# Kernel optimization log

Hardware: AMD Instinct MI355X
Metric: run time of the kernel (lower is better)

Reference implementation:

```python
import jax, jax.numpy as jnp
import numpy as np
import math

HID = 1024      # opt.hidden_dim
NH = 8          # num_heads (hardcoded in module)
HD = HID // NH  # indiv_head_dim = 128
G = 16          # opt.group_num
GD = HID // G   # per-group dim = 64
FEAT = 1024     # opt.feature_dim
V, T = 8, 256   # videos x frames
E = 256         # number of events
L = 64          # max_att_len (clip window)
N = 384         # expanded event_num
WAVE = 10000.0


def setup_inputs() -> dict:
    rng = np.random.RandomState(0)
    key = jax.random.key(0)
    ks = jax.random.split(key, 12)

    feats = jax.random.normal(ks[0], (V * T, FEAT), dtype=jnp.float32)

    # ragged clip spans -> dense gather idx + mask (the Basic_Encoder loop)
    starts = rng.randint(0, V * T - L, size=(E,))
    clip_gather_idx = jnp.asarray(starts[:, None] + np.arange(L)[None, :], dtype=jnp.int32)
    lens = rng.randint(8, L + 1, size=(E,))
    clip_mask = jnp.asarray((np.arange(L)[None, :] < lens[:, None]).astype(np.float32))

    # event_seq_idx expansion: rows -> event ids, block-diagonal mask
    expand_idx = jnp.asarray(rng.randint(0, E, size=(N,)), dtype=jnp.int32)
    block_mask = np.zeros((N, N), dtype=np.float32)
    pos = 0
    while pos < N:
        b = min(int(rng.randint(8, 49)), N - pos)
        block_mask[pos:pos + b, pos:pos + b] = 1.0
        pos += b
    block_mask = jnp.asarray(block_mask)

    # normalized timestamps (start < end, in [0,1])
    s = rng.uniform(0.0, 0.8, size=(N, 1)).astype(np.float32)
    e = s + rng.uniform(0.02, 0.2, size=(N, 1)).astype(np.float32)
    bbox = jnp.asarray(np.concatenate([s, e], axis=1))

    sc = 1.0 / math.sqrt(HID)
    scd = 1.0 / math.sqrt(HD)
    Wpre = jax.random.normal(ks[1], (HID, FEAT), dtype=jnp.float32) * sc
    bpre = jnp.zeros((HID,), dtype=jnp.float32)
    Wq = jax.random.normal(ks[2], (NH, HD, HD), dtype=jnp.float32) * scd
    bq = jnp.zeros((NH, HD), dtype=jnp.float32)
    Wk = jax.random.normal(ks[3], (NH, HD, HD), dtype=jnp.float32) * scd
    bk = jnp.zeros((NH, HD), dtype=jnp.float32)
    Wv = jax.random.normal(ks[4], (NH, HD, HD), dtype=jnp.float32) * scd
    bv = jnp.zeros((NH, HD), dtype=jnp.float32)
    Wp1 = jax.random.normal(ks[5], (HID, HID), dtype=jnp.float32) * sc
    bp1 = jnp.zeros((HID,), dtype=jnp.float32)
    Wp2 = jax.random.normal(ks[6], (G, HID), dtype=jnp.float32) * sc
    bp2 = jnp.zeros((G,), dtype=jnp.float32)

    return dict(feats=feats, clip_gather_idx=clip_gather_idx, clip_mask=clip_mask,
                expand_idx=expand_idx, block_mask=block_mask, bbox=bbox,
                Wpre=Wpre, bpre=bpre, Wq=Wq, bq=bq, Wk=Wk, bk=bk, Wv=Wv, bv=bv,
                Wp1=Wp1, bp1=bp1, Wp2=Wp2, bp2=bp2)


def _sinusoid(x, feat_dim):
    # extract_position_embedding: x [..., P] -> [..., P*feat_dim/2*2] reshaped to feat_dim per row
    fr = jnp.arange(feat_dim // 4, dtype=x.dtype)
    dim_mat = WAVE ** (4.0 / feat_dim * fr)              # (feat_dim/4,)
    div = (100.0 * x)[..., None] / dim_mat               # (..., P, feat_dim/4)
    return jnp.concatenate([jnp.sin(div), jnp.cos(div)], axis=-1)


def reference(feats, clip_gather_idx, clip_mask, expand_idx, block_mask, bbox,
              Wpre, bpre, Wq, bq, Wk, bk, Wv, bv, Wp1, bp1, Wp2, bp2):
    # ---- clip-level pooling (Basic_Encoder.get_clip_level_feats + mean) ----
    clip_feats = feats[clip_gather_idx] * clip_mask[..., None]          # (E, L, FEAT)
    event = clip_feats.sum(1) / (clip_mask.sum(1, keepdims=True) + 1e-5)  # (E, FEAT)
    event = jax.nn.relu(event @ Wpre.T + bpre)                          # pre_map (dropout=eval)

    # ---- expand per event_seq_idx ----
    x = event[expand_idx]                                               # (N, HID)

    # ---- 8 per-head q/k/v maps, split into G groups ----
    xh = x.reshape(N, NH, HD)
    def proj(W, b):
        y = jnp.einsum('nhd,hed->nhe', xh, W) + b                       # (N, NH, HD)
        return y.reshape(N, G, GD).transpose(1, 0, 2)                   # (G, N, GD)
    q, k, v = proj(Wq, bq), proj(Wk, bk), proj(Wv, bv)
    scores = jnp.einsum('gnd,gmd->gnm', q, k) / math.sqrt(GD)           # (G, N, N)

    # ---- position branch: pairwise geometric relation bias ----
    start, end = bbox[:, 0:1], bbox[:, 1:2]                             # (N,1)
    center = 0.5 * (start + end)
    length = jnp.maximum(end - start, 0.1)
    dc = (center - center.T) / length
    dl = jnp.log(length.T / length)
    pm = jnp.stack([dc, dl], axis=2)                                    # (N, N, 2)
    emb = _sinusoid(pm, HID).reshape(N, N, HID)                         # (N, N, HID)
    pos = jax.nn.relu(emb @ Wp1.T + bp1)                                # pair_pos_fc1
    pos = jax.nn.relu(pos @ Wp2.T + bp2)                                # pair_pos_fc2 -> (N, N, G)
    pos_bias = jnp.log(jnp.clip(pos, 1e-6)).transpose(2, 0, 1)          # (G, N, N)

    scores = scores + pos_bias
    scores = jnp.where(block_mask[None] > 0, scores, -1e9)
    att = jax.nn.softmax(scores, axis=-1)                               # (G, N, N)
    out = jnp.einsum('gnm,gmd->gnd', att, v)                            # (G, N, GD)
    out = out.transpose(1, 0, 2).reshape(N, HID)

    # ---- per-event 100-dim temporal position embedding ----
    e100 = _sinusoid(bbox, 100).reshape(N, 100)

    return jnp.concatenate([x, out, e100], axis=-1)                     # (N, 2*HID + 100)
```

## Files before the change

### kernel.cpp

```cpp
#include <hip/hip_runtime.h>
#include <hip/hip_bf16.h>

typedef unsigned short u16;
typedef _Float16 h16;
typedef __attribute__((ext_vector_type(8))) h16 h8;
typedef __attribute__((ext_vector_type(8))) u16 us8;
typedef __attribute__((ext_vector_type(4))) float f4;

#define DEVFN __device__ __forceinline__

constexpr int kN = 384;
constexpr int kL = 64;
constexpr int kMaxP = kN * 48;
constexpr int kOutCols = 2148;
constexpr float kLoScale = 2048.f;
constexpr float kLoInv = 1.f / 2048.f;

union HU { h16 h; u16 u; };
DEVFN u16 f2h(float f) { HU c; c.h = (h16)f; return c.u; }
DEVFN float h2f(u16 b) { HU c; c.u = b; return (float)c.h; }

DEVFN f4 mfma16h(h8 a, h8 b, f4 c) {
  return __builtin_amdgcn_mfma_f32_16x16x32_f16(a, b, c, 0, 0, 0);
}

DEVFN h8 pack8h(float4 x0, float4 x1) {
  h8 a;
  a[0] = (h16)x0.x; a[1] = (h16)x0.y; a[2] = (h16)x0.z; a[3] = (h16)x0.w;
  a[4] = (h16)x1.x; a[5] = (h16)x1.y; a[6] = (h16)x1.z; a[7] = (h16)x1.w;
  return a;
}

DEVFN void fsincos(float ang, float& s, float& c) {
  float n = rintf(ang * 0.15915494309189535f);
  const float PI2_HI = 6.2831854820251465f;
  const float PI2_LO = -1.7484555e-07f;
  float r = fmaf(-n, PI2_HI, ang);
  r = fmaf(-n, PI2_LO, r);
  s = __sinf(r);
  c = __cosf(r);
}

__global__ __launch_bounds__(256) void k_front(
    const float* __restrict__ Wp1, u16* __restrict__ W1H, u16* __restrict__ W1L,
    const float* __restrict__ Wp2, u16* __restrict__ W2H, u16* __restrict__ W2L,
    const float* __restrict__ Wpre, u16* __restrict__ WpreH,
    const float* __restrict__ Wq, u16* __restrict__ WqH,
    const float* __restrict__ Wk, u16* __restrict__ WkH,
    const float* __restrict__ Wv, u16* __restrict__ WvH,
    const float* __restrict__ bm, int* __restrict__ row_start, int* __restrict__ row_len,
    const float* __restrict__ feats, const int* __restrict__ gidx,
    const float* __restrict__ cmask, float* __restrict__ mean) {
  int bid = blockIdx.x, t = threadIdx.x;
  if (bid < 512) {
    const int nW1 = 1048576, nW2 = 16384, nPre = 1048576, nQ = 131072;
    const int tot = nW1 + nW2 + nPre + 3 * nQ;
    for (int i = bid * 256 + t; i < tot; i += 512 * 256) {
      if (i < nW1) {
        float x = Wp1[i]; u16 h = f2h(x);
        W1H[i] = h; W1L[i] = f2h((x - h2f(h)) * kLoScale);
      } else if (i < nW1 + nW2) {
        int j = i - nW1; float x = Wp2[j]; u16 h = f2h(x);
        W2H[j] = h; W2L[j] = f2h((x - h2f(h)) * kLoScale);
      } else if (i < nW1 + nW2 + nPre) {
        int j = i - nW1 - nW2; WpreH[j] = f2h(Wpre[j]);
      } else {
        int j = i - nW1 - nW2 - nPre;
        int a = j / nQ, r = j % nQ;
        const float* s = (a == 0) ? Wq : (a == 1) ? Wk : Wv;
        u16* d = (a == 0) ? WqH : (a == 1) ? WkH : WvH;
        d[r] = f2h(s[r]);
      }
    }
  } else if (bid < 608) {
    int w = t >> 6, lane = t & 63;
    int i = (bid - 512) * 4 + w;
    int mn = kN, mx = -1;
    #pragma unroll
    for (int jb = 0; jb < kN; jb += 64) {
      float m = bm[(size_t)i * kN + jb + lane];
      if (m > 0.f) { mn = min(mn, jb + lane); mx = max(mx, jb + lane); }
    }
    #pragma unroll
    for (int off = 32; off > 0; off >>= 1) {
      mn = min(mn, __shfl_xor(mn, off));
      mx = max(mx, __shfl_xor(mx, off));
    }
    if (lane == 0) { row_start[i] = mn; row_len[i] = mx - mn + 1; }
  } else {
    int e = bid - 608;
    float4 a = {0.f, 0.f, 0.f, 0.f};
    float ms = 0.f;
    for (int l = 0; l < kL; ++l) {
      float m = cmask[e * kL + l];
      ms += m;
      if (m > 0.f) {
        float4 v = *(const float4*)(feats + (size_t)gidx[e * kL + l] * 1024 + t * 4);
        a.x += v.x; a.y += v.y; a.z += v.z; a.w += v.w;
      }
    }
    float inv = 1.f / (ms + 1e-5f);
    float4 o = {a.x * inv, a.y * inv, a.z * inv, a.w * inv};
    *(float4*)(mean + (size_t)e * 1024 + t * 4) = o;
  }
}

__global__ __launch_bounds__(64) void k_scan(const int* __restrict__ row_len,
                                             int* __restrict__ row_off,
                                             int* __restrict__ Ptr) {
  int lane = threadIdx.x;
  int s[6], tot = 0;
  #pragma unroll
  for (int r = 0; r < 6; ++r) { s[r] = tot; tot += row_len[lane * 6 + r]; }
  int run = tot;
  #pragma unroll
  for (int off = 1; off < 64; off <<= 1) {
    int u = __shfl_up(run, off);
    if (lane >= off) run += u;
  }
  int excl = run - tot;
  #pragma unroll
  for (int r = 0; r < 6; ++r) row_off[lane * 6 + r] = excl + s[r];
  if (lane == 63) Ptr[0] = excl + tot;
}

__global__ __launch_bounds__(64) void k_fill(const int* __restrict__ row_start,
                                             const int* __restrict__ row_len,
                                             const int* __restrict__ row_off,
                                             int* __restrict__ pair_i,
                                             int* __restrict__ pair_j) {
  int i = blockIdx.x, lane = threadIdx.x;
  int s = row_start[i], len = row_len[i], off = row_off[i];
  if (lane < len) { pair_i[off + lane] = i; pair_j[off + lane] = s + lane; }
}

__global__ __launch_bounds__(256) void k_mid(
    const int* __restrict__ Ptr, const int* __restrict__ row_start,
    const int* __restrict__ row_off, const float* __restrict__ bbox,
    u16* __restrict__ ehi, u16* __restrict__ elo,
    const float* __restrict__ mean, const u16* __restrict__ WpreH,
    const float* __restrict__ bpre, float* __restrict__ event) {
  int bid = blockIdx.x, t = threadIdx.x;
  if (bid < 9216) {
    __shared__ double As[16], Bs[16];
    __shared__ int roff[384], rstart[384];
    const double kCd = -13.287712379549449 / 256.0;
    if (t < 16) As[t] = exp2(kCd * (double)(t * 16));
    else if (t < 32) Bs[t - 16] = exp2(kCd * (double)(t - 16));
    for (int k = t; k < 384; k += 256) { roff[k] = row_off[k]; rstart[k] = row_start[k]; }
    __syncthreads();
    int P = Ptr[0];
    int Pc = (P + 127) & ~127;
    int p = bid * 2 + (t >> 7);
    if (p >= Pc) return;
    int kb = (t & 127) * 8;
    size_t o = (size_t)p * 1024 + kb;
    us8 vh, vl;
    if (p >= P) {
      #pragma unroll
      for (int j = 0; j < 8; ++j) { vh[j] = 0; vl[j] = 0; }
      *(us8*)(ehi + o) = vh;
      *(us8*)(elo + o) = vl;
      return;
    }
    int lo = 0, hi = 383;
    while (lo < hi) { int md = (lo + hi + 1) >> 1; if (roff[md] <= p) lo = md; else hi = md - 1; }
    int pi = lo, pj = rstart[lo] + (p - roff[lo]);
    double s0 = bbox[pi * 2], e0 = bbox[pi * 2 + 1];
    double s1 = bbox[pj * 2], e1 = bbox[pj * 2 + 1];
    double li = fmax(e0 - s0, 0.1), lj = fmax(e1 - s1, 0.1);
    double x = (kb < 512) ? (0.5 * (s0 + e0) - 0.5 * (s1 + e1)) / li : log(lj / li);
    double x100 = 100.0 * x;
    bool iscos = (kb >> 8) & 1;
    int f0 = kb & 255;
    const double INV2PI = 0.15915494309189535;
    const double TWOPI  = 6.283185307179586;
    #pragma unroll
    for (int j = 0; j < 8; ++j) {
      int f = f0 + j;
      double ang = x100 * (As[f >> 4] * Bs[f & 15]);
      double nn = rint(ang * INV2PI);
      float rf = (float)fma(-nn, TWOPI, ang);
      float sv = iscos ? __cosf(rf) : __sinf(rf);
      u16 h = f2h(sv);
      vh[j] = h;
      vl[j] = f2h((sv - h2f(h)) * kLoScale);
    }
    *(us8*)(ehi + o) = vh;
    *(us8*)(elo + o) = vl;
  } else {
    int b2 = bid - 9216;
    int mt = b2 >> 4, nc = b2 & 15;
    int w = t >> 6, lane = t & 63, lr = lane & 15, lg = lane >> 4;
    f4 acc = {};
    const float* arow = mean + (size_t)(mt * 16 + lr) * 1024;
    #pragma unroll
    for (int ks = 0; ks < 32; ++ks) {
      const float* ap = arow + ks * 32 + lg * 8;
      h8 a = pack8h(*(const float4*)ap, *(const float4*)(ap + 4));
      h8 b = *(const h8*)(WpreH + (size_t)(nc * 64 + w * 16 + lr) * 1024 + ks * 32 + lg * 8);
      acc = mfma16h(a, b, acc);
    }
    #pragma unroll
    for (int r = 0; r < 4; ++r) {
      int row = mt * 16 + lg * 4 + r, cn = nc * 64 + w * 16 + lr;
      event[(size_t)row * 1024 + cn] = fmaxf(acc[r] + bpre[cn], 0.f);
    }
  }
}

__global__ __launch_bounds__(256, 2) void k_main(
    const int* __restrict__ Ptr, const u16* __restrict__ ehi, const u16* __restrict__ elo,
    const u16* __restrict__ W1h, const u16* __restrict__ W1l, const float* __restrict__ bias1,
    const u16* __restrict__ W2h, const u16* __restrict__ W2l, float* __restrict__ z2part,
    const float* __restrict__ event, const int* __restrict__ eidx,
    const u16* __restrict__ WqH, const float* __restrict__ bq,
    const u16* __restrict__ WkH, const float* __restrict__ bk,
    const u16* __restrict__ WvH, const float* __restrict__ bv,
    float* __restrict__ qb, float* __restrict__ kbuf, float* __restrict__ vbuf) {
  __shared__ u16 lds[2][4][4096];
  int bid = blockIdx.x, tid = threadIdx.x;
  if (bid < 1152) {
    int P = Ptr[0];
    int mb = bid % 144, nb = bid / 144;
    if (mb * 128 >= P) return;
    int w = tid >> 6, lane = tid & 63;
    int lr = lane & 15, lg = lane >> 4;
    int srow[2], scol[2];
    #pragma unroll
    for (int cc = 0; cc < 2; ++cc) {
      int c = w * 2 + cc;
      int d = c * 1024 + lane * 16;
      int b = d ^ (((((d >> 6) & 3)) ^ ((d >> 8) & 3)) << 4);
      srow[cc] = b >> 6;
      scol[cc] = b & 63;
    }
    const u16* planes[4] = {ehi, elo, W1h, W1l};
    int rb0 = mb * 128, rb1 = nb * 128;
    auto stage = [&](int buf, int k0) {
      #pragma unroll
      for (int t = 0; t < 4; ++t) {
        int rbase = (t < 2) ? rb0 : rb1;
        #pragma unroll
        for (int cc = 0; cc < 2; ++cc) {
          int c = w * 2 + cc;
          const char* src = (const char*)(planes[t] + (size_t)(rbase + srow[cc]) * 1024 + k0) + scol[cc];
          char* dst = (char*)&lds[buf][t][0] + c * 1024;
          __builtin_amdgcn_global_load_lds(
              (const __attribute__((address_space(1))) char*)src,
              (__attribute__((address_space(3))) char*)dst, 16, 0, 0);
        }
      }
    };
    stage(0, 0);
    f4 aH[4][4] = {}, aL[4][4] = {};
    int wm = (w >> 1) * 64, wn = (w & 1) * 64;
    int sl = (lg ^ (lr & 3) ^ ((lr >> 2) & 3)) << 4;
    __syncthreads();
    for (int kt = 0; kt < 32; ++kt) {
      int cur = kt & 1;
      if (kt < 31) stage(cur ^ 1, (kt + 1) * 32);
      h8 ah[4], al[4], bh[4], bl[4];
      #pragma unroll
      for (int mt = 0; mt < 4; ++mt) {
        int ad = (wm + mt * 16 + lr) * 64 + sl;
        ah[mt] = *(const h8*)((const char*)&lds[cur][0][0] + ad);
        al[mt] = *(const h8*)((const char*)&lds[cur][1][0] + ad);
      }
      #pragma unroll
      for (int nt = 0; nt < 4; ++nt) {
        int ad = (wn + nt * 16 + lr) * 64 + sl;
        bh[nt] = *(const h8*)((const char*)&lds[cur][2][0] + ad);
        bl[nt] = *(const h8*)((const char*)&lds[cur][3][0] + ad);
      }
      #pragma unroll
      for (int mt = 0; mt < 4; ++mt)
        #pragma unroll
        for (int nt = 0; nt < 4; ++nt) {
          aH[mt][nt] = mfma16h(ah[mt], bh[nt], aH[mt][nt]);
          aL[mt][nt] = mfma16h(al[mt], bh[nt], aL[mt][nt]);
          aL[mt][nt] = mfma16h(ah[mt], bl[nt], aL[mt][nt]);
        }
      __syncthreads();
    }
    float* zq = (float*)&lds[0][0][0] + w * 4096;
    #pragma unroll
    for (int mt = 0; mt < 4; ++mt)
      #pragma unroll
      for (int nt = 0; nt < 4; ++nt)
        #pragma unroll
        for (int r = 0; r < 4; ++r) {
          int pl = mt * 16 + lg * 4 + r;
          int nl = nt * 16 + lr;
          float z1 = aH[mt][nt][r] + aL[mt][nt][r] * kLoInv + bias1[nb * 128 + wn + nl];
          zq[pl * 64 + (nl ^ ((pl & 7) << 3))] = fmaxf(z1, 0.f);
        }
    __syncthreads();
    f4 c2h[4], c2l[4];
    #pragma unroll
    for (int i = 0; i < 4; ++i) { c2h[i] = f4{}; c2l[i] = f4{}; }
    #pragma unroll
    for (int mt2 = 0; mt2 < 4; ++mt2) {
      #pragma unroll
      for (int kc = 0; kc < 2; ++kc) {
        int pl = mt2 * 16 + lr;
        int n0 = kc * 32 + lg * 8;
        const float* rp = zq + pl * 64 + (n0 ^ ((pl & 7) << 3));
        float4 v0 = *(const float4*)rp;
        float4 v1 = *(const float4*)(rp + 4);
        h8 ah2, al2;
        #pragma unroll
        for (int j = 0; j < 4; ++j) {
          h16 h0 = (h16)v0[j]; ah2[j] = h0;     al2[j] = (h16)((v0[j] - (float)h0) * kLoScale);
          h16 h1 = (h16)v1[j]; ah2[4 + j] = h1; al2[4 + j] = (h16)((v1[j] - (float)h1) * kLoScale);
        }
        int ng = nb * 128 + wn + n0;
        h8 bh2 = *(const h8*)(W2h + lr * 1024 + ng);
        h8 bl2 = *(const h8*)(W2l + lr * 1024 + ng);
        c2h[mt2] = mfma16h(ah2, bh2, c2h[mt2]);
        c2l[mt2] = mfma16h(al2, bh2, c2l[mt2]);
        c2l[mt2] = mfma16h(ah2, bl2, c2l[mt2]);
      }
    }
    int slice = nb * 2 + (w & 1);
    #pragma unroll
    for (int mt2 = 0; mt2 < 4; ++mt2)
      #pragma unroll
      for (int r = 0; r < 4; ++r) {
        int p = mb * 128 + wm + mt2 * 16 + lg * 4 + r;
        z2part[((size_t)slice * kMaxP + p) * 16 + lr] = c2h[mt2][r] + c2l[mt2][r] * kLoInv;
      }
  } else {
    int b2 = bid - 1152;
    int z = b2 / 192, r2 = b2 % 192, mt = r2 >> 3, h = r2 & 7;
    int w = tid >> 6, lane = tid & 63, lr = lane & 15, lg = lane >> 4;
    const u16* W = (z == 0) ? WqH : (z == 1) ? WkH : WvH;
    const float* bias = (z == 0) ? bq : (z == 1) ? bk : bv;
    float* out = (z == 0) ? qb : (z == 1) ? kbuf : vbuf;
    int row = mt * 16 + lr;
    const float* arow = event + (size_t)eidx[row] * 1024 + h * 128;
    f4 acc[2] = {};
    #pragma unroll
    for (int ks = 0; ks < 4; ++ks) {
      const float* ap = arow + ks * 32 + lg * 8;
      h8 a = pack8h(*(const float4*)ap, *(const float4*)(ap + 4));
      #pragma unroll
      for (int n2 = 0; n2 < 2; ++n2) {
        int nt = w * 2 + n2;
        h8 b = *(const h8*)(W + h * 16384 + (nt * 16 + lr) * 128 + ks * 32 + lg * 8);
        acc[n2] = mfma16h(a, b, acc[n2]);
      }
    }
    #pragma unroll
    for (int n2 = 0; n2 < 2; ++n2)
      #pragma unroll
      for (int r = 0; r < 4; ++r) {
        int rn = mt * 16 + lg * 4 + r, e = (w * 2 + n2) * 16 + lr;
        out[(size_t)rn * 1024 + h * 128 + e] = acc[n2][r] + bias[h * 128 + e];
      }
  }
}

__global__ __launch_bounds__(256) void k_back(
    const int* __restrict__ Ptr, const float* __restrict__ z2part,
    const float* __restrict__ bias2, float* __restrict__ bias_o,
    const float* __restrict__ event, const int* __restrict__ eidx,
    const float* __restrict__ bbox, float* __restrict__ dout) {
  int bid = blockIdx.x, t = threadIdx.x;
  if (bid < 1152) {
    int P = Ptr[0];
    int idx = bid * 256 + t;
    if (idx >= P * 16) return;
    int g = idx & 15;
    float s = bias2[g];
    #pragma unroll
    for (int b = 0; b < 16; ++b) s += z2part[(size_t)b * kMaxP * 16 + idx];
    bias_o[idx] = logf(fmaxf(s, 1e-6f));
  } else {
    int i = bid - 1152;
    const float* er = event + (size_t)eidx[i] * 1024;
    float* orow = dout + (size_t)i * kOutCols;
    for (int c = t; c < 1024; c += 256) orow[c] = er[c];
    if (t < 100) {
      int qq = t / 25, f = t % 25;
      float x = bbox[i * 2 + (qq >> 1)];
      float ang = 100.f * x * exp2f((float)f * (-13.287712379549449f * 0.04f));
      float sv, cv;
      fsincos(ang, sv, cv);
      orow[2048 + t] = (qq & 1) ? cv : sv;
    }
  }
}

__global__ __launch_bounds__(64) void k_att(const float* __restrict__ q,
                                            const float* __restrict__ kk,
                                            const float* __restrict__ vv,
                                            const float* __restrict__ bias,
                                            const int* __restrict__ row_start,
                                            const int* __restrict__ row_len,
                                            const int* __restrict__ row_off,
                                            float* __restrict__ dout) {
  int i = blockIdx.x, g = blockIdx.y, lane = threadIdx.x;
  int s = row_start[i], L = row_len[i], pb = row_off[i];
  __shared__ float qs[64];
  __shared__ float att[64];
  qs[lane] = q[(size_t)i * 1024 + g * 64 + lane];
  __syncthreads();
  bool valid = lane < L;
  const float* kr = kk + (size_t)(s + (valid ? lane : 0)) * 1024 + g * 64;
  float sc = 0.f;
  #pragma unroll
  for (int dt = 0; dt < 16; ++dt) {
    float4 kv = *(const float4*)(kr + dt * 4);
    sc += qs[dt * 4 + 0] * kv.x + qs[dt * 4 + 1] * kv.y +
          qs[dt * 4 + 2] * kv.z + qs[dt * 4 + 3] * kv.w;
  }
  sc = valid ? (sc * 0.125f + bias[(size_t)(pb + lane) * 16 + g]) : -3.0e38f;
  float mx = sc;
  #pragma unroll
  for (int off = 32; off > 0; off >>= 1) mx = fmaxf(mx, __shfl_xor(mx, off));
  float pe = valid ? __expf(sc - mx) : 0.f;
  float sm = pe;
  #pragma unroll
  for (int off = 32; off > 0; off >>= 1) sm += __shfl_xor(sm, off);
  att[lane] = pe / sm;
  __syncthreads();
  float o = 0.f;
  const float* vb = vv + (size_t)s * 1024 + g * 64 + lane;
  for (int jl = 0; jl < L; ++jl) o += att[jl] * vb[(size_t)jl * 1024];
  dout[(size_t)i * kOutCols + 1024 + g * 64 + lane] = o;
}

__global__ __launch_bounds__(256) void k_pos(
    const int* __restrict__ Ptr, const int* __restrict__ pair_i,
    const int* __restrict__ pair_j, const float* __restrict__ bbox,
    const u16* __restrict__ W1h, const u16* __restrict__ W1l,
    const float* __restrict__ bias1,
    const u16* __restrict__ W2h, const u16* __restrict__ W2l,
    const float* __restrict__ bias2, float* __restrict__ bias_out) {
  int P = Ptr[0];
  int base0 = blockIdx.x * 64;
  if (base0 >= P) return;
  int w = threadIdx.x >> 6, l = threadIdx.x & 63;
  int lr = l & 15, lg = l >> 4;
  int base = base0 + w * 16;
  int p = base + lr;
  bool valid = p < P;
  int pi = valid ? pair_i[p] : 0;
  int pj = valid ? pair_j[p] : 0;
  double s0 = bbox[pi * 2], e0 = bbox[pi * 2 + 1];
  double s1 = bbox[pj * 2], e1 = bbox[pj * 2 + 1];
  double li = fmax(e0 - s0, 0.1), lj = fmax(e1 - s1, 0.1);
  double dcd = (0.5 * (s0 + e0) - 0.5 * (s1 + e1)) / li;
  double dld = log(lj / li);
  const double kCd = -13.287712379549449 / 256.0;
  double r1  = exp2(kCd);
  double r32 = exp2(kCd * 32.0);
  double pb0 = exp2(kCd * (double)(lg * 8));
  const double INV2PI = 0.15915494309189535;
  const double TWOPI  = 6.283185307179586;
  h8 eh[32], el[32];
  #pragma unroll
  for (int hx = 0; hx < 2; ++hx) {
    double x100 = 100.0 * (hx ? dld : dcd);
    double pch = pb0;
    #pragma unroll
    for (int ksl = 0; ksl < 8; ++ksl) {
      double pp = pch;
      #pragma unroll
      for (int j = 0; j < 8; ++j) {
        double ang = x100 * pp;
        double nn = rint(ang * INV2PI);
        float rf = (float)fma(-nn, TWOPI, ang);
        float sv = __sinf(rf), cv = __cosf(rf);
        h16 sh = (h16)sv, ch = (h16)cv;
        eh[hx * 16 + ksl][j] = sh;
        el[hx * 16 + ksl][j] = (h16)((sv - (float)sh) * kLoScale);
        eh[hx * 16 + 8 + ksl][j] = ch;
        el[hx * 16 + 8 + ksl][j] = (h16)((cv - (float)ch) * kLoScale);
        pp *= r1;
      }
      pch *= r32;
    }
  }
  __shared__ float p1f[4][16 * 64];
  char* myp1 = (char*)p1f[w];
  f4 acc2 = {}, acc2l = {};
  for (int nc = 0; nc < 16; ++nc) {
    f4 accH[4] = {}, accL[4] = {};
    #pragma unroll
    for (int ks = 0; ks < 32; ++ks) {
      #pragma unroll
      for (int nt = 0; nt < 4; ++nt) {
        size_t boff = (size_t)(nc * 64 + nt * 16 + lr) * 1024 + ks * 32 + lg * 8;
        h8 bh = *(const h8*)(W1h + boff);
        h8 bl = *(const h8*)(W1l + boff);
        accH[nt] = mfma16h(eh[ks], bh, accH[nt]);
        accL[nt] = mfma16h(el[ks], bh, accL[nt]);
        accL[nt] = mfma16h(eh[ks], bl, accL[nt]);
      }
    }
    __syncthreads();
    #pragma unroll
    for (int nt = 0; nt < 4; ++nt)
      #pragma unroll
      for (int r = 0; r < 4; ++r) {
        int m = lg * 4 + r, n = nt * 16 + lr;
        float z1 = accH[nt][r] + accL[nt][r] * kLoInv + bias1[nc * 64 + n];
        int byte = ((m * 64 + n) * 4) ^ ((m & 7) << 4);
        *(float*)(myp1 + byte) = fmaxf(z1, 0.f);
      }
    __syncthreads();
    #pragma unroll
    for (int hf = 0; hf < 2; ++hf) {
      int kb = hf * 32 + lg * 8;
      int b0 = ((lr * 64 + kb) * 4) ^ ((lr & 7) << 4);
      int b1 = ((lr * 64 + kb + 4) * 4) ^ ((lr & 7) << 4);
      float4 x0 = *(const float4*)(myp1 + b0);
      float4 x1 = *(const float4*)(myp1 + b1);
      h8 ah, al;
      #pragma unroll
      for (int j = 0; j < 4; ++j) {
        h16 h0 = (h16)x0[j];
        ah[j] = h0; al[j] = (h16)((x0[j] - (float)h0) * kLoScale);
        h16 h1 = (h16)x1[j];
        ah[4 + j] = h1; al[4 + j] = (h16)((x1[j] - (float)h1) * kLoScale);
      }
      h8 bh = *(const h8*)(W2h + lr * 1024 + nc * 64 + kb);
      h8 bl = *(const h8*)(W2l + lr * 1024 + nc * 64 + kb);
      acc2  = mfma16h(ah, bh, acc2);
      acc2l = mfma16h(al, bh, acc2l);
      acc2l = mfma16h(ah, bl, acc2l);
    }
  }
  #pragma unroll
  for (int r = 0; r < 4; ++r) {
    int m = lg * 4 + r;
    int pp = base + m;
    if (pp < P) {
      float v0 = acc2[r] + acc2l[r] * kLoInv + bias2[lr];
      bias_out[(size_t)pp * 16 + lr] = logf(fmaxf(v0, 1e-6f));
    }
  }
}

extern "C" void kernel_launch(void* const* d_in, const int* in_sizes, int n_in,
                              void* d_out, int out_size, void* d_ws, size_t ws_size,
                              hipStream_t stream) {
  const float* feats = (const float*)d_in[0];
  const int*   gidx  = (const int*)d_in[1];
  const float* cmask = (const float*)d_in[2];
  const int*   eidx  = (const int*)d_in[3];
  const float* bmask = (const float*)d_in[4];
  const float* bbox  = (const float*)d_in[5];
  const float* Wpre  = (const float*)d_in[6];
  const float* bpre  = (const float*)d_in[7];
  const float* Wq    = (const float*)d_in[8];
  const float* bq    = (const float*)d_in[9];
  const float* Wk    = (const float*)d_in[10];
  const float* bk    = (const float*)d_in[11];
  const float* Wv    = (const float*)d_in[12];
  const float* bv    = (const float*)d_in[13];
  const float* Wp1   = (const float*)d_in[14];
  const float* bp1   = (const float*)d_in[15];
  const float* Wp2   = (const float*)d_in[16];
  const float* bp2   = (const float*)d_in[17];

  char* ws = (char*)d_ws;
  size_t off = 0;
  auto alloc = [&](size_t bytes) {
    char* r = ws + off;
    off += (bytes + 255) & ~(size_t)255;
    return r;
  };
  u16* W1H   = (u16*)alloc((size_t)1048576 * 2);
  u16* W1L   = (u16*)alloc((size_t)1048576 * 2);
  u16* W2H   = (u16*)alloc((size_t)16384 * 2);
  u16* W2L   = (u16*)alloc((size_t)16384 * 2);
  u16* WpreH = (u16*)alloc((size_t)1048576 * 2);
  u16* WqH   = (u16*)alloc((size_t)131072 * 2);
  u16* WkH   = (u16*)alloc((size_t)131072 * 2);
  u16* WvH   = (u16*)alloc((size_t)131072 * 2);
  float* mean  = (float*)alloc((size_t)256 * 1024 * 4);
  float* event = (float*)alloc((size_t)256 * 1024 * 4);
  float* qb    = (float*)alloc((size_t)384 * 1024 * 4);
  float* kb    = (float*)alloc((size_t)384 * 1024 * 4);
  float* vb    = (float*)alloc((size_t)384 * 1024 * 4);
  int* row_start = (int*)alloc(kN * 4);
  int* row_len   = (int*)alloc(kN * 4);
  int* row_off   = (int*)alloc(kN * 4);
  int* Ptr       = (int*)alloc(256);
  int* pair_i    = (int*)alloc((size_t)kMaxP * 4);
  int* pair_j    = (int*)alloc((size_t)kMaxP * 4);
  float* bias_o  = (float*)alloc((size_t)kMaxP * 16 * 4);
  u16* ehi      = (u16*)alloc((size_t)kMaxP * 1024 * 2);
  u16* elo      = (u16*)alloc((size_t)kMaxP * 1024 * 2);
  float* z2part = (float*)alloc((size_t)16 * kMaxP * 16 * 4);
  bool fast = (off <= ws_size);

  k_front<<<864, 256, 0, stream>>>(Wp1, W1H, W1L, Wp2, W2H, W2L, Wpre, WpreH,
                                   Wq, WqH, Wk, WkH, Wv, WvH,
                                   bmask, row_start, row_len,
                                   feats, gidx, cmask, mean);
  k_scan<<<1, 64, 0, stream>>>(row_len, row_off, Ptr);

  if (fast) {
    k_mid<<<9472, 256, 0, stream>>>(Ptr, row_start, row_off, bbox, ehi, elo,
                                    mean, WpreH, bpre, event);
    k_main<<<1728, 256, 0, stream>>>(Ptr, ehi, elo, W1H, W1L, bp1, W2H, W2L, z2part,
                                     event, eidx, WqH, bq, WkH, bk, WvH, bv, qb, kb, vb);
    k_back<<<1536, 256, 0, stream>>>(Ptr, z2part, bp2, bias_o, event, eidx, bbox,
                                     (float*)d_out);
  } else {
    k_mid<<<9472, 256, 0, stream>>>(Ptr, row_start, row_off, bbox, ehi, elo,
                                    mean, WpreH, bpre, event);
    k_fill<<<kN, 64, 0, stream>>>(row_start, row_len, row_off, pair_i, pair_j);
    k_pos<<<kMaxP / 64, 256, 0, stream>>>(Ptr, pair_i, pair_j, bbox, W1H, W1L, bp1,
                                          W2H, W2L, bp2, bias_o);
    k_main<<<1728, 256, 0, stream>>>(Ptr, ehi, elo, W1H, W1L, bp1, W2H, W2L, z2part,
                                     event, eidx, WqH, bq, WkH, bk, WvH, bv, qb, kb, vb);
    k_back<<<1536, 256, 0, stream>>>(Ptr, z2part, bp2, bias_o, event, eidx, bbox,
                                     (float*)d_out);
  }
  k_att<<<dim3(kN, 16), 64, 0, stream>>>(qb, kb, vb, bias_o, row_start, row_len, row_off,
                                         (float*)d_out);
}
```

Baseline: 177.2 us.

## Replace split-K partial buffer with atomic accumulation and fold reduction into attention

The 16-slice z2part partial-sum buffer and the separate k_back reduction kernel are removed. k_main now atomically adds its fc2 partials into a zeroed bias_acc buffer, which extra k_front blocks clear. k_att applies bias2 and the log clamp on the fly, and it absorbs the event-row and temporal-embedding output writes, so one launch and a large intermediate read/write disappear. It also reorders k_main's block index so N-blocks are adjacent, and makes k_mid exit early before its LDS setup. The cost is atomic contention on bias_acc (16 adds per element) and non-deterministic float summation order.

Measured after the change: 161.6 us. 1.1x faster.

```diff
diff --git a/kernel.cpp b/kernel.cpp
--- a/kernel.cpp
+++ b/kernel.cpp
@@ -50,7 +50,8 @@
     const float* __restrict__ Wv, u16* __restrict__ WvH,
     const float* __restrict__ bm, int* __restrict__ row_start, int* __restrict__ row_len,
     const float* __restrict__ feats, const int* __restrict__ gidx,
-    const float* __restrict__ cmask, float* __restrict__ mean) {
+    const float* __restrict__ cmask, float* __restrict__ mean,
+    float* __restrict__ bias_acc) {
   int bid = blockIdx.x, t = threadIdx.x;
   if (bid < 512) {
     const int nW1 = 1048576, nW2 = 16384, nPre = 1048576, nQ = 131072;
@@ -87,7 +88,7 @@
       mx = max(mx, __shfl_xor(mx, off));
     }
     if (lane == 0) { row_start[i] = mn; row_len[i] = mx - mn + 1; }
-  } else {
+  } else if (bid < 864) {
     int e = bid - 608;
     float4 a = {0.f, 0.f, 0.f, 0.f};
     float ms = 0.f;
@@ -102,6 +103,10 @@
     float inv = 1.f / (ms + 1e-5f);
     float4 o = {a.x * inv, a.y * inv, a.z * inv, a.w * inv};
     *(float4*)(mean + (size_t)e * 1024 + t * 4) = o;
+  } else {
+    float4 z = {0.f, 0.f, 0.f, 0.f};
+    for (int i4 = (bid - 864) * 256 + t; i4 < kMaxP * 16 / 4; i4 += 48 * 256)
+      *(float4*)(bias_acc + (size_t)i4 * 4) = z;
   }
 }
 
@@ -142,6 +147,9 @@
     const float* __restrict__ bpre, float* __restrict__ event) {
   int bid = blockIdx.x, t = threadIdx.x;
   if (bid < 9216) {
+    int P = Ptr[0];
+    int Pc = (P + 127) & ~127;
+    if (bid * 2 >= Pc) return;
     __shared__ double As[16], Bs[16];
     __shared__ int roff[384], rstart[384];
     const double kCd = -13.287712379549449 / 256.0;
@@ -149,10 +157,7 @@
     else if (t < 32) Bs[t - 16] = exp2(kCd * (double)(t - 16));
     for (int k = t; k < 384; k += 256) { roff[k] = row_off[k]; rstart[k] = row_start[k]; }
     __syncthreads();
-    int P = Ptr[0];
-    int Pc = (P + 127) & ~127;
     int p = bid * 2 + (t >> 7);
-    if (p >= Pc) return;
     int kb = (t & 127) * 8;
     size_t o = (size_t)p * 1024 + kb;
     us8 vh, vl;
@@ -212,17 +217,19 @@
 __global__ __launch_bounds__(256, 2) void k_main(
     const int* __restrict__ Ptr, const u16* __restrict__ ehi, const u16* __restrict__ elo,
     const u16* __restrict__ W1h, const u16* __restrict__ W1l, const float* __restrict__ bias1,
-    const u16* __restrict__ W2h, const u16* __restrict__ W2l, float* __restrict__ z2part,
+    const u16* __restrict__ W2h, const u16* __restrict__ W2l, float* __restrict__ bias_acc,
     const float* __restrict__ event, const int* __restrict__ eidx,
     const u16* __restrict__ WqH, const float* __restrict__ bq,
     const u16* __restrict__ WkH, const float* __restrict__ bk,
     const u16* __restrict__ WvH, const float* __restrict__ bv,
-    float* __restrict__ qb, float* __restrict__ kbuf, float* __restrict__ vbuf) {
+    float* __restrict__ qb, float* __restrict__ kbuf, float* __restrict__ vbuf,
+    int pos_on) {
   __shared__ u16 lds[2][4][4096];
   int bid = blockIdx.x, tid = threadIdx.x;
   if (bid < 1152) {
+    if (!pos_on) return;
     int P = Ptr[0];
-    int mb = bid % 144, nb = bid / 144;
+    int nb = bid & 7, mb = bid >> 3;
     if (mb * 128 >= P) return;
     int w = tid >> 6, lane = tid & 63;
     int lr = lane & 15, lg = lane >> 4;
@@ -322,13 +329,13 @@
         c2l[mt2] = mfma16h(ah2, bl2, c2l[mt2]);
       }
     }
-    int slice = nb * 2 + (w & 1);
     #pragma unroll
     for (int mt2 = 0; mt2 < 4; ++mt2)
       #pragma unroll
       for (int r = 0; r < 4; ++r) {
         int p = mb * 128 + wm + mt2 * 16 + lg * 4 + r;
-        z2part[((size_t)slice * kMaxP + p) * 16 + lr] = c2h[mt2][r] + c2l[mt2][r] * kLoInv;
+        if (p < P)
+          atomicAdd(&bias_acc[(size_t)p * 16 + lr], c2h[mt2][r] + c2l[mt2][r] * kLoInv);
       }
   } else {
     int b2 = bid - 1152;
@@ -361,27 +368,29 @@
   }
 }
 
-__global__ __launch_bounds__(256) void k_back(
-    const int* __restrict__ Ptr, const float* __restrict__ z2part,
-    const float* __restrict__ bias2, float* __restrict__ bias_o,
-    const float* __restrict__ event, const int* __restrict__ eidx,
-    const float* __restrict__ bbox, float* __restrict__ dout) {
-  int bid = blockIdx.x, t = threadIdx.x;
-  if (bid < 1152) {
-    int P = Ptr[0];
-    int idx = bid * 256 + t;
-    if (idx >= P * 16) return;
-    int g = idx & 15;
-    float s = bias2[g];
-    #pragma unroll
-    for (int b = 0; b < 16; ++b) s += z2part[(size_t)b * kMaxP * 16 + idx];
-    bias_o[idx] = logf(fmaxf(s, 1e-6f));
-  } else {
-    int i = bid - 1152;
+__global__ __launch_bounds__(64) void k_att(const float* __restrict__ q,
+                                            const float* __restrict__ kk,
+                                            const float* __restrict__ vv,
+                                            const float* __restrict__ bias_acc,
+                                            const float* __restrict__ bias2,
+                                            const int* __restrict__ row_start,
+                                            const int* __restrict__ row_len,
+                                            const int* __restrict__ row_off,
+                                            const float* __restrict__ event,
+                                            const int* __restrict__ eidx,
+                                            const float* __restrict__ bbox,
+                                            float* __restrict__ dout) {
+  int bid = blockIdx.x, lane = threadIdx.x;
+  if (bid >= 6144) {
+    int i = bid - 6144;
     const float* er = event + (size_t)eidx[i] * 1024;
     float* orow = dout + (size_t)i * kOutCols;
-    for (int c = t; c < 1024; c += 256) orow[c] = er[c];
-    if (t < 100) {
+    #pragma unroll
+    for (int it = 0; it < 4; ++it) {
+      int c = lane * 4 + it * 256;
+      *(float4*)(orow + c) = *(const float4*)(er + c);
+    }
+    for (int t = lane; t < 100; t += 64) {
       int qq = t / 25, f = t % 25;
       float x = bbox[i * 2 + (qq >> 1)];
       float ang = 100.f * x * exp2f((float)f * (-13.287712379549449f * 0.04f));
@@ -389,18 +398,9 @@
       fsincos(ang, sv, cv);
       orow[2048 + t] = (qq & 1) ? cv : sv;
     }
-  }
-}
-
-__global__ __launch_bounds__(64) void k_att(const float* __restrict__ q,
-                                            const float* __restrict__ kk,
-                                            const float* __restrict__ vv,
-                                            const float* __restrict__ bias,
-                                            const int* __restrict__ row_start,
-                                            const int* __restrict__ row_len,
-                                            const int* __restrict__ row_off,
-                                            float* __restrict__ dout) {
-  int i = blockIdx.x, g = blockIdx.y, lane = threadIdx.x;
+    return;
+  }
+  int i = bid >> 4, g = bid & 15;
   int s = row_start[i], L = row_len[i], pb = row_off[i];
   __shared__ float qs[64];
   __shared__ float att[64];
@@ -415,7 +415,13 @@
     sc += qs[dt * 4 + 0] * kv.x + qs[dt * 4 + 1] * kv.y +
           qs[dt * 4 + 2] * kv.z + qs[dt * 4 + 3] * kv.w;
   }
-  sc = valid ? (sc * 0.125f + bias[(size_t)(pb + lane) * 16 + g]) : -3.0e38f;
+  int pidx = min(pb + lane, kMaxP - 1);
+  float pbias = 0.f;
+  if (valid) {
+    float zs = bias_acc[(size_t)pidx * 16 + g] + bias2[g];
+    pbias = logf(fmaxf(zs, 1e-6f));
+  }
+  sc = valid ? (sc * 0.125f + pbias) : -3.0e38f;
   float mx = sc;
   #pragma unroll
   for (int off = 32; off > 0; off >>= 1) mx = fmaxf(mx, __shfl_xor(mx, off));
@@ -437,7 +443,7 @@
     const u16* __restrict__ W1h, const u16* __restrict__ W1l,
     const float* __restrict__ bias1,
     const u16* __restrict__ W2h, const u16* __restrict__ W2l,
-    const float* __restrict__ bias2, float* __restrict__ bias_out) {
+    float* __restrict__ bias_acc) {
   int P = Ptr[0];
   int base0 = blockIdx.x * 64;
   if (base0 >= P) return;
@@ -537,10 +543,8 @@
   for (int r = 0; r < 4; ++r) {
     int m = lg * 4 + r;
     int pp = base + m;
-    if (pp < P) {
-      float v0 = acc2[r] + acc2l[r] * kLoInv + bias2[lr];
-      bias_out[(size_t)pp * 16 + lr] = logf(fmaxf(v0, 1e-6f));
-    }
+    if (pp < P)
+      bias_acc[(size_t)pp * 16 + lr] = acc2[r] + acc2l[r] * kLoInv;
   }
 }
 
@@ -592,36 +596,31 @@
   int* Ptr       = (int*)alloc(256);
   int* pair_i    = (int*)alloc((size_t)kMaxP * 4);
   int* pair_j    = (int*)alloc((size_t)kMaxP * 4);
-  float* bias_o  = (float*)alloc((size_t)kMaxP * 16 * 4);
+  float* bias_acc = (float*)alloc((size_t)kMaxP * 16 * 4);
   u16* ehi      = (u16*)alloc((size_t)kMaxP * 1024 * 2);
   u16* elo      = (u16*)alloc((size_t)kMaxP * 1024 * 2);
-  float* z2part = (float*)alloc((size_t)16 * kMaxP * 16 * 4);
   bool fast = (off <= ws_size);
 
-  k_front<<<864, 256, 0, stream>>>(Wp1, W1H, W1L, Wp2, W2H, W2L, Wpre, WpreH,
+  k_front<<<912, 256, 0, stream>>>(Wp1, W1H, W1L, Wp2, W2H, W2L, Wpre, WpreH,
                                    Wq, WqH, Wk, WkH, Wv, WvH,
                                    bmask, row_start, row_len,
-                                   feats, gidx, cmask, mean);
+                                   feats, gidx, cmask, mean, bias_acc);
   k_scan<<<1, 64, 0, stream>>>(row_len, row_off, Ptr);
 
   if (fast) {
     k_mid<<<9472, 256, 0, stream>>>(Ptr, row_start, row_off, bbox, ehi, elo,
                                     mean, WpreH, bpre, event);
-    k_main<<<1728, 256, 0, stream>>>(Ptr, ehi, elo, W1H, W1L, bp1, W2H, W2L, z2part,
-                                     event, eidx, WqH, bq, WkH, bk, WvH, bv, qb, kb, vb);
-    k_back<<<1536, 256, 0, stream>>>(Ptr, z2part, bp2, bias_o, event, eidx, bbox,
-                                     (float*)d_out);
+    k_main<<<1728, 256, 0, stream>>>(Ptr, ehi, elo, W1H, W1L, bp1, W2H, W2L, bias_acc,
+                                     event, eidx, WqH, bq, WkH, bk, WvH, bv, qb, kb, vb, 1);
   } else {
     k_mid<<<9472, 256, 0, stream>>>(Ptr, row_start, row_off, bbox, ehi, elo,
                                     mean, WpreH, bpre, event);
     k_fill<<<kN, 64, 0, stream>>>(row_start, row_len, row_off, pair_i, pair_j);
     k_pos<<<kMaxP / 64, 256, 0, stream>>>(Ptr, pair_i, pair_j, bbox, W1H, W1L, bp1,
-                                          W2H, W2L, bp2, bias_o);
-    k_main<<<1728, 256, 0, stream>>>(Ptr, ehi, elo, W1H, W1L, bp1, W2H, W2L, z2part,
-                                     event, eidx, WqH, bq, WkH, bk, WvH, bv, qb, kb, vb);
-    k_back<<<1536, 256, 0, stream>>>(Ptr, z2part, bp2, bias_o, event, eidx, bbox,
-                                     (float*)d_out);
-  }
-  k_att<<<dim3(kN, 16), 64, 0, stream>>>(qb, kb, vb, bias_o, row_start, row_len, row_off,
-                                         (float*)d_out);
-}
+                                          W2H, W2L, bias_acc);
+    k_main<<<1728, 256, 0, stream>>>(Ptr, ehi, elo, W1H, W1L, bp1, W2H, W2L, bias_acc,
+                                     event, eidx, WqH, bq, WkH, bk, WvH, bv, qb, kb, vb, 0);
+  }
+  k_att<<<6528, 64, 0, stream>>>(qb, kb, vb, bias_acc, bp2, row_start, row_len, row_off,
+                                 event, eidx, bbox, (float*)d_out);
+}
```
